# Optimization experiments

Hardware: AMD Instinct MI355X
Metric: run time of the kernel (lower is better)

## Reference

```python
import jax, jax.numpy as jnp
import numpy as np
import math

B, C, H, W = 8, 64, 256, 256
E, NH = 256, 8
HD = E // NH  # 32


def get_coords(h, w):
    xx, yy = jnp.meshgrid(jnp.arange(h, dtype=jnp.float32), jnp.arange(w, dtype=jnp.float32), indexing='ij')
    return jnp.stack((xx.reshape(-1), yy.reshape(-1)), axis=-1)  # [N, 2]


def setup_inputs() -> dict:
    key = jax.random.key(0)
    ks = jax.random.split(key, 12)
    def xavier(k, shape):
        fan_out, fan_in = shape
        a = math.sqrt(6.0 / (fan_in + fan_out))
        return jax.random.uniform(k, shape, jnp.float32, -a, a)
    x = jax.random.normal(ks[0], (B, C, H, W), jnp.float32)
    z = jax.random.normal(ks[1], (B, C), jnp.float32)
    pos = jax.random.uniform(ks[2], (B, NH, 2), jnp.float32) * (H - 1)
    Wq = xavier(ks[3], (E, C)); bq = jnp.zeros((E,), jnp.float32)
    Wk = xavier(ks[4], (E, C)); bk = jnp.zeros((E,), jnp.float32)
    Wv = xavier(ks[5], (E, C)); bv = jnp.zeros((E,), jnp.float32)
    Wp = xavier(ks[6], (HD, 2)); bp = jax.random.uniform(ks[7], (HD,), jnp.float32, -1.0, 1.0) / math.sqrt(2.0)
    return {"x": x, "z": z, "pos": pos, "Wq": Wq, "bq": bq, "Wk": Wk, "bk": bk,
            "Wv": Wv, "bv": bv, "Wp": Wp, "bp": bp}


def reference(x, z, pos, Wq, bq, Wk, bk, Wv, bv, Wp, bp):
    b, c, h, w = x.shape
    n = h * w
    x_flat = x.reshape(b, c, n).transpose(0, 2, 1)          # [B, N, C]
    pos_grid = get_coords(h, w)                              # [N, 2]
    q = (z @ Wq.T + bq).reshape(b, NH, HD)                   # [B, H, hd]
    k = (x_flat @ Wk.T + bk).reshape(b, n, NH, HD)           # [B, N, H, hd]
    # relative-position modulation of keys
    rel = pos_grid[None, :, None, :] - pos[:, None, :, :]    # [B, N, H, 2]
    qxk = rel @ Wp.T + bp                                    # [B, N, H, hd]
    k = k * qxk
    v = x_flat @ Wv.T + bv                                   # [B, N, E]
    attn_logits = jnp.einsum('bhc,bnhc->bnh', q, k) / math.sqrt(HD)
    attention = jax.nn.softmax(attn_logits, axis=1)          # softmax over N
    pos_out = jnp.einsum('bnh,nx->bhx', attention, pos_grid) # [B, H, 2]
    values = jnp.einsum('bnh,bnc->bhc', attention, v)        # [B, H, E]
    return (values, pos_out)
```

## Files before the change

kernel.cpp:

```cpp
#include <hip/hip_runtime.h>

#define NN    65536
#define NSUB  128
#define NBLK  (NN/NSUB)

typedef short bf16x8 __attribute__((ext_vector_type(8)));
typedef float f32x4v __attribute__((ext_vector_type(4)));
typedef unsigned short ushort_t;
typedef unsigned int uint_t;

#define XSTR   72
#define XHI_B  0
#define XLO_B  18432
#define LGA_B  18432
#define LGSTR  28
#define PSTR   136
#define RED_B  36864
#define SMEM_BYTES 37056

#define WTHI_B  0
#define WTLO_B  32768
#define CJ_B    65536
#define PM_B    66304
#define PL_B    197376
#define PSP_B   328448
#define PSX_B   590592
#define Q_B     8979200
#define QSTR    68

__device__ __forceinline__ uint_t bf16_rne_bits(float f) {
  uint_t u = __float_as_uint(f);
  return (u + 0x7FFFu + ((u >> 16) & 1u)) >> 16;
}
template <int CTRL>
__device__ __forceinline__ float dpp_add(float x) {
  int t = __builtin_amdgcn_update_dpp(0, __float_as_int(x), CTRL, 0xf, 0xf, false);
  return x + __int_as_float(t);
}
template <int CTRL>
__device__ __forceinline__ float dpp_maxs(float x) {
  int t = __builtin_amdgcn_update_dpp((int)0xFF800000u, __float_as_int(x), CTRL, 0xf, 0xf, false);
  return fmaxf(x, __int_as_float(t));
}
__device__ __forceinline__ float wave_sum(float x) {
  x = dpp_add<0x111>(x); x = dpp_add<0x112>(x); x = dpp_add<0x114>(x);
  x = dpp_add<0x118>(x); x = dpp_add<0x142>(x); x = dpp_add<0x143>(x);
  return __int_as_float(__builtin_amdgcn_readlane(__float_as_int(x), 63));
}
__device__ __forceinline__ float wave_max(float x) {
  x = dpp_maxs<0x111>(x); x = dpp_maxs<0x112>(x); x = dpp_maxs<0x114>(x);
  x = dpp_maxs<0x118>(x); x = dpp_maxs<0x142>(x); x = dpp_maxs<0x143>(x);
  return __int_as_float(__builtin_amdgcn_readlane(__float_as_int(x), 63));
}

__global__ __launch_bounds__(64) void prep_kernel(
    const float* __restrict__ z,  const float* __restrict__ Wq, const float* __restrict__ bq,
    const float* __restrict__ Wk, const float* __restrict__ bk,
    const float* __restrict__ Wp, const float* __restrict__ bp,
    ushort_t* __restrict__ WThi, ushort_t* __restrict__ WTlo, float* __restrict__ Cj)
{
  const int h = blockIdx.x, b = blockIdx.y, t = threadIdx.x;
  __shared__ float q[32];
  if (t < 32) {
    const int e = h*32 + t;
    float a = bq[e];
    const float* zr = z + b*64;
    const float* wr = Wq + e*64;
    #pragma unroll 8
    for (int c = 0; c < 64; ++c) a += zr[c]*wr[c];
    q[t] = a;
  }
  __syncthreads();
  const int c = t;
  float w[3] = {0.f, 0.f, 0.f};
  #pragma unroll 4
  for (int hd = 0; hd < 32; ++hd) {
    const float qk = q[hd] * Wk[(h*32+hd)*64 + c];
    w[0] += qk * bp[hd];
    w[1] += qk * Wp[hd*2+0];
    w[2] += qk * Wp[hd*2+1];
  }
  #pragma unroll
  for (int j = 0; j < 3; ++j) {
    const int coeff = h*3 + j;
    const uint_t hb = bf16_rne_bits(w[j]);
    const float  fh = __uint_as_float(hb << 16);
    const uint_t lb = bf16_rne_bits(w[j] - fh);
    WThi[(b*32 + coeff)*64 + c] = (ushort_t)hb;
    WTlo[(b*32 + coeff)*64 + c] = (ushort_t)lb;
  }
  if (h == 0) {
    #pragma unroll
    for (int r = 0; r < 8; ++r) {
      WThi[(b*32 + 24 + r)*64 + c] = 0;
      WTlo[(b*32 + 24 + r)*64 + c] = 0;
    }
  }
  if (t < 3) {
    float s = 0.f;
    for (int hd = 0; hd < 32; ++hd) {
      const float m = (t == 0) ? bp[hd] : Wp[hd*2 + (t-1)];
      s += q[hd] * m * bk[h*32+hd];
    }
    Cj[b*24 + h*3 + t] = s;
  }
}

__global__ __launch_bounds__(128, 2) void main_kernel(
    const float* __restrict__ x, const float* __restrict__ pos,
    const ushort_t* __restrict__ WThi, const ushort_t* __restrict__ WTlo,
    const float* __restrict__ Cj,
    float* __restrict__ Pm, float* __restrict__ Pl,
    float* __restrict__ Psp, float* __restrict__ Psx)
{
  extern __shared__ char smc[];
  ushort_t* xhi = (ushort_t*)(smc + XHI_B);
  float*    lga = (float*)(smc + LGA_B);
  float*    red = (float*)(smc + RED_B);
  const int t   = threadIdx.x;
  const int blk = blockIdx.x;
  const int b   = blockIdx.y;
  const int n0  = blk * NSUB;
  const int wid = t >> 6, lid = t & 63;
  const int c0  = lid & 15, q4 = lid >> 4;

  bf16x8 bh[2][2], bl[2][2];
  {
    const ushort_t* wtb_h = WThi + b*2048;
    const ushort_t* wtb_l = WTlo + b*2048;
    #pragma unroll
    for (int nt = 0; nt < 2; ++nt)
      #pragma unroll
      for (int ks = 0; ks < 2; ++ks) {
        const int off = (nt*16 + c0)*64 + ks*32 + q4*8;
        bh[nt][ks] = *(const bf16x8*)(wtb_h + off);
        bl[nt][ks] = *(const bf16x8*)(wtb_l + off);
      }
  }

  {
    const float* xg = x + (size_t)b*64*NN + n0 + t;
    float v[64];
    #pragma unroll
    for (int i = 0; i < 64; ++i) v[i] = xg[(size_t)i*NN];
    #pragma unroll
    for (int cc = 0; cc < 4; ++cc) {
      uint_t hb[16], lb[16];
      #pragma unroll
      for (int i = 0; i < 16; ++i) {
        const float f = v[cc*16+i];
        hb[i] = bf16_rne_bits(f);
        lb[i] = __float_as_uint(f - __uint_as_float(hb[i] << 16)) >> 16;
      }
      uint4 H0 = make_uint4(hb[0]|(hb[1]<<16), hb[2]|(hb[3]<<16), hb[4]|(hb[5]<<16), hb[6]|(hb[7]<<16));
      uint4 H1 = make_uint4(hb[8]|(hb[9]<<16), hb[10]|(hb[11]<<16), hb[12]|(hb[13]<<16), hb[14]|(hb[15]<<16));
      uint4 L0 = make_uint4(lb[0]|(lb[1]<<16), lb[2]|(lb[3]<<16), lb[4]|(lb[5]<<16), lb[6]|(lb[7]<<16));
      uint4 L1 = make_uint4(lb[8]|(lb[9]<<16), lb[10]|(lb[11]<<16), lb[12]|(lb[13]<<16), lb[14]|(lb[15]<<16));
      char* dh = smc + XHI_B + t*144 + cc*32;
      char* dl = smc + XLO_B + t*144 + cc*32;
      *(uint4*)(dh)      = H0;  *(uint4*)(dh + 16) = H1;
      *(uint4*)(dl)      = L0;  *(uint4*)(dl + 16) = L1;
    }
  }

  float cj[24];
  {
    const float* cjp = Cj + b*24;
    #pragma unroll
    for (int k = 0; k < 24; ++k) cj[k] = cjp[k];
  }
  const int gx = blk >> 1;
  float rxh[8], py[8];
  #pragma unroll
  for (int h = 0; h < 8; ++h) {
    rxh[h] = (float)gx - pos[(b*8+h)*2 + 0];
    py[h]  = pos[(b*8+h)*2 + 1];
  }

  __syncthreads();

  f32x4v acc[4][2];
  #pragma unroll
  for (int mt = 0; mt < 4; ++mt) { acc[mt][0] = (f32x4v)0.f; acc[mt][1] = (f32x4v)0.f; }
  {
    const int mrow0 = wid*64;
    #pragma unroll
    for (int mt = 0; mt < 4; ++mt) {
      const int row = mrow0 + mt*16 + c0;
      const ushort_t* ph = xhi + row*XSTR + q4*8;
      const ushort_t* pl = (ushort_t*)(smc + XLO_B) + row*XSTR + q4*8;
      bf16x8 ah0 = *(const bf16x8*)(ph);
      bf16x8 ah1 = *(const bf16x8*)(ph + 32);
      bf16x8 al0 = *(const bf16x8*)(pl);
      bf16x8 al1 = *(const bf16x8*)(pl + 32);
      #pragma unroll
      for (int nt = 0; nt < 2; ++nt) {
        f32x4v a = acc[mt][nt];
        a = __builtin_amdgcn_mfma_f32_16x16x32_bf16(ah0, bh[nt][0], a, 0, 0, 0);
        a = __builtin_amdgcn_mfma_f32_16x16x32_bf16(ah1, bh[nt][1], a, 0, 0, 0);
        a = __builtin_amdgcn_mfma_f32_16x16x32_bf16(ah0, bl[nt][0], a, 0, 0, 0);
        a = __builtin_amdgcn_mfma_f32_16x16x32_bf16(ah1, bl[nt][1], a, 0, 0, 0);
        a = __builtin_amdgcn_mfma_f32_16x16x32_bf16(al0, bh[nt][0], a, 0, 0, 0);
        a = __builtin_amdgcn_mfma_f32_16x16x32_bf16(al1, bh[nt][1], a, 0, 0, 0);
        acc[mt][nt] = a;
      }
    }
  }
  __syncthreads();

  {
    const int mrow0 = wid*64;
    #pragma unroll
    for (int mt = 0; mt < 4; ++mt)
      #pragma unroll
      for (int r = 0; r < 4; ++r) {
        const int prow = mrow0 + mt*16 + q4*4 + r;
        lga[prow*LGSTR + c0] = acc[mt][0][r];
        if (c0 < 8) lga[prow*LGSTR + 16 + c0] = acc[mt][1][r];
      }
  }
  __syncthreads();

  float a24[24];
  {
    const float4* ap = (const float4*)(lga + t*LGSTR);
    #pragma unroll
    for (int r = 0; r < 6; ++r) *(float4*)(a24 + 4*r) = ap[r];
  }
  const float tf = (float)(((blk & 1) << 7) + t);
  float lg[8];
  #pragma unroll
  for (int h = 0; h < 8; ++h) {
    const float a0 = a24[h*3+0] + cj[h*3+0];
    const float a1 = a24[h*3+1] + cj[h*3+1];
    const float a2 = a24[h*3+2] + cj[h*3+2];
    lg[h] = (a0 + rxh[h]*a1 + (tf - py[h])*a2) * 0.17677669529663687f;
  }

  #pragma unroll
  for (int h = 0; h < 8; ++h) {
    const float m = wave_max(lg[h]);
    if (lid == 0) red[h*2 + wid] = m;
  }
  __syncthreads();

  float p[8];
  #pragma unroll
  for (int h = 0; h < 8; ++h) {
    const float M = fmaxf(red[h*2+0], red[h*2+1]);
    p[h] = __expf(lg[h] - M);
  }

  {
    ushort_t* pls = (ushort_t*)(smc + LGA_B);
    #pragma unroll
    for (int h = 0; h < 8; ++h) {
      const uint_t hb = bf16_rne_bits(p[h]);
      const float  hf = __uint_as_float(hb << 16);
      const uint_t lb = __float_as_uint(p[h] - hf) >> 16;
      pls[h*PSTR + t]       = (ushort_t)hb;
      pls[(h+8)*PSTR + t]   = (ushort_t)lb;
    }
  }

  #pragma unroll
  for (int h = 0; h < 8; ++h) {
    const float sp  = wave_sum(p[h]);
    const float spj = wave_sum(p[h] * tf);
    if (lid == 0) { red[16 + h*2 + wid] = sp; red[32 + h*2 + wid] = spj; }
  }
  __syncthreads();

  if (t < 8) {
    const int base = (b*NBLK + blk)*8 + t;
    const float M  = fmaxf(red[t*2+0], red[t*2+1]);
    const float L  = red[16+t*2+0] + red[16+t*2+1];
    const float SJ = red[32+t*2+0] + red[32+t*2+1];
    Pm[base] = M;
    Pl[base] = L;
    Psp[base*2+0] = (float)gx * L;
    Psp[base*2+1] = SJ;
  }

  {
    const ushort_t* pls = (const ushort_t*)(smc + LGA_B);
    bf16x8 afr[4];
    #pragma unroll
    for (int ks = 0; ks < 4; ++ks)
      afr[ks] = *(const bf16x8*)(pls + c0*PSTR + ks*32 + q4*8);

    f32x4v accB0 = (f32x4v)0.f, accB1 = (f32x4v)0.f;
    const int chbase = wid*32 + c0;
    #pragma unroll
    for (int ks = 0; ks < 4; ++ks) {
      const ushort_t* xcol = xhi + (ks*32 + q4*8)*XSTR + chbase;
      bf16x8 b0, b1;
      #pragma unroll
      for (int i = 0; i < 8; ++i) {
        b0[i] = (short)xcol[i*XSTR];
        b1[i] = (short)xcol[i*XSTR + 16];
      }
      accB0 = __builtin_amdgcn_mfma_f32_16x16x32_bf16(afr[ks], b0, accB0, 0, 0, 0);
      accB1 = __builtin_amdgcn_mfma_f32_16x16x32_bf16(afr[ks], b1, accB1, 0, 0, 0);
    }

    const size_t pb64 = ((size_t)(b*NBLK + blk))*8*64;
    #pragma unroll
    for (int r = 0; r < 4; ++r) {
      const float o0 = __shfl_xor(accB0[r], 32, 64);
      const float o1 = __shfl_xor(accB1[r], 32, 64);
      if (q4 < 2) {
        const int h = q4*4 + r;
        const int c = wid*32 + c0;
        Psx[pb64 + h*64 + c]      = accB0[r] + o0;
        Psx[pb64 + h*64 + c + 16] = accB1[r] + o1;
      }
    }
  }
}

__global__ __launch_bounds__(256) void reduce1_kernel(
    const float* __restrict__ Pm, const float* __restrict__ Pl,
    const float* __restrict__ Psp, const float* __restrict__ Psx,
    float* __restrict__ Q)
{
  const int g = blockIdx.x, h = blockIdx.y, b = blockIdx.z, t = threadIdx.x;
  __shared__ float al[64];
  __shared__ float mgs;
  __shared__ float sums[3];
  __shared__ float sxl[256];
  const int base = (b*NBLK + g*64)*8 + h;

  float m_t = -1e30f;
  if (t < 64) {
    m_t = Pm[base + t*8];
    float mm = m_t;
    #pragma unroll
    for (int off = 32; off >= 1; off >>= 1) mm = fmaxf(mm, __shfl_xor(mm, off, 64));
    if (t == 0) mgs = mm;
  }
  __syncthreads();
  const float Mg = mgs;
  if (t < 64) {
    const float a = __expf(m_t - Mg);
    al[t] = a;
    float lt = Pl[base + t*8] * a;
    float sx = Psp[(base + t*8)*2 + 0] * a;
    float sy = Psp[(base + t*8)*2 + 1] * a;
    #pragma unroll
    for (int off = 32; off >= 1; off >>= 1) {
      lt += __shfl_xor(lt, off, 64);
      sx += __shfl_xor(sx, off, 64);
      sy += __shfl_xor(sy, off, 64);
    }
    if (t == 0) { sums[0] = lt; sums[1] = sx; sums[2] = sy; }
  }
  __syncthreads();
  {
    const int c = t & 63, g2 = t >> 6;
    float acc = 0.f;
    #pragma unroll
    for (int i = 0; i < 16; ++i) {
      const int k = g2*16 + i;
      acc += al[k] * Psx[(size_t)(base + k*8)*64 + c];
    }
    sxl[g2*64 + c] = acc;
  }
  __syncthreads();
  float* q = Q + ((b*8 + h)*8 + g)*QSTR;
  if (t < 64) q[4+t] = sxl[t] + sxl[64+t] + sxl[128+t] + sxl[192+t];
  if (t == 0) { q[0] = Mg; q[1] = sums[0]; q[2] = sums[1]; q[3] = sums[2]; }
}

__global__ __launch_bounds__(64) void reduce2_kernel(
    const float* __restrict__ Q, const float* __restrict__ Wv, const float* __restrict__ bv,
    float* __restrict__ out)
{
  const int h = blockIdx.x, b = blockIdx.y, t = threadIdx.x;
  __shared__ float qm[8], bl[8], l8[8], sx8[8], sy8[8];
  __shared__ float SXs[64];
  const float* qb = Q + ((b*8 + h)*8)*QSTR;

  if (t < 8) qm[t] = qb[t*QSTR + 0];
  __syncthreads();
  float M = qm[0];
  #pragma unroll
  for (int g = 1; g < 8; ++g) M = fmaxf(M, qm[g]);
  if (t < 8) {
    const float be = __expf(qm[t] - M);
    bl[t]  = be;
    l8[t]  = be * qb[t*QSTR + 1];
    sx8[t] = be * qb[t*QSTR + 2];
    sy8[t] = be * qb[t*QSTR + 3];
  }
  __syncthreads();
  float L = 0.f;
  #pragma unroll
  for (int g = 0; g < 8; ++g) L += l8[g];
  const float invL = 1.0f / L;
  {
    float s = 0.f;
    #pragma unroll
    for (int g = 0; g < 8; ++g) s += bl[g] * qb[g*QSTR + 4 + t];
    SXs[t] = s * invL;
  }
  __syncthreads();

  #pragma unroll
  for (int r = 0; r < 4; ++r) {
    const int e = t + 64*r;
    float v = bv[e];
    const float* wvr = Wv + e*64;
    #pragma unroll 8
    for (int c = 0; c < 64; ++c) v += wvr[c] * SXs[c];
    out[(b*8 + h)*256 + e] = v;
  }
  if (t == 0) {
    float spx = 0.f, spy = 0.f;
    #pragma unroll
    for (int g = 0; g < 8; ++g) { spx += sx8[g]; spy += sy8[g]; }
    out[16384 + (b*8 + h)*2 + 0] = spx * invL;
    out[16384 + (b*8 + h)*2 + 1] = spy * invL;
  }
}

extern "C" void kernel_launch(void* const* d_in, const int* in_sizes, int n_in,
                              void* d_out, int out_size, void* d_ws, size_t ws_size,
                              hipStream_t stream)
{
  const float* x   = (const float*)d_in[0];
  const float* z   = (const float*)d_in[1];
  const float* pos = (const float*)d_in[2];
  const float* Wq  = (const float*)d_in[3];
  const float* bq  = (const float*)d_in[4];
  const float* Wk  = (const float*)d_in[5];
  const float* bk  = (const float*)d_in[6];
  const float* Wv  = (const float*)d_in[7];
  const float* bv  = (const float*)d_in[8];
  const float* Wp  = (const float*)d_in[9];
  const float* bp  = (const float*)d_in[10];
  float* out = (float*)d_out;
  char*  wsb = (char*)d_ws;

  ushort_t* WThi = (ushort_t*)(wsb + WTHI_B);
  ushort_t* WTlo = (ushort_t*)(wsb + WTLO_B);
  float* Cj  = (float*)(wsb + CJ_B);
  float* Pm  = (float*)(wsb + PM_B);
  float* Pl  = (float*)(wsb + PL_B);
  float* Psp = (float*)(wsb + PSP_B);
  float* Psx = (float*)(wsb + PSX_B);
  float* Q   = (float*)(wsb + Q_B);

  prep_kernel   <<<dim3(8,8),    64,  0,          stream>>>(z, Wq, bq, Wk, bk, Wp, bp, WThi, WTlo, Cj);
  main_kernel   <<<dim3(NBLK,8), 128, SMEM_BYTES, stream>>>(x, pos, WThi, WTlo, Cj, Pm, Pl, Psp, Psx);
  reduce1_kernel<<<dim3(8,8,8),  256, 0,          stream>>>(Pm, Pl, Psp, Psx, Q);
  reduce2_kernel<<<dim3(8,8),    64,  0,          stream>>>(Q, Wv, bv, out);
}
```

Measured before the change: 237.7 us.

## Split main kernel work across 256 threads per block instead of 128

Doubles the threads per block of the main kernel. Each pixel's 64 channels are now loaded by two threads, each covering 32 channels, and the four waves split the GEMM rows, the heads and the output channel tiles between them. This cuts per-thread register pressure (64 loaded floats become 32) and raises the number of loads in flight, to hide the latency of the strided global reads of x. The launch bound now requests 4 blocks of 256, which caps registers per thread and could cause spills.

```diff
diff --git a/kernel.cpp b/kernel.cpp
--- a/kernel.cpp
+++ b/kernel.cpp
@@ -106,7 +106,7 @@
   }
 }
 
-__global__ __launch_bounds__(128, 2) void main_kernel(
+__global__ __launch_bounds__(256, 4) void main_kernel(
     const float* __restrict__ x, const float* __restrict__ pos,
     const ushort_t* __restrict__ WThi, const ushort_t* __restrict__ WTlo,
     const float* __restrict__ Cj,
@@ -123,6 +123,9 @@
   const int n0  = blk * NSUB;
   const int wid = t >> 6, lid = t & 63;
   const int c0  = lid & 15, q4 = lid >> 4;
+  const int px  = t & 127;
+  const int hgrp = t >> 7;
+  const int half = wid & 1;
 
   bf16x8 bh[2][2], bl[2][2];
   {
@@ -139,12 +142,12 @@
   }
 
   {
-    const float* xg = x + (size_t)b*64*NN + n0 + t;
-    float v[64];
-    #pragma unroll
-    for (int i = 0; i < 64; ++i) v[i] = xg[(size_t)i*NN];
-    #pragma unroll
-    for (int cc = 0; cc < 4; ++cc) {
+    const float* xg = x + (size_t)b*64*NN + (size_t)hgrp*32*NN + n0 + px;
+    float v[32];
+    #pragma unroll
+    for (int i = 0; i < 32; ++i) v[i] = xg[(size_t)i*NN];
+    #pragma unroll
+    for (int cc = 0; cc < 2; ++cc) {
       uint_t hb[16], lb[16];
       #pragma unroll
       for (int i = 0; i < 16; ++i) {
@@ -156,36 +159,37 @@
       uint4 H1 = make_uint4(hb[8]|(hb[9]<<16), hb[10]|(hb[11]<<16), hb[12]|(hb[13]<<16), hb[14]|(hb[15]<<16));
       uint4 L0 = make_uint4(lb[0]|(lb[1]<<16), lb[2]|(lb[3]<<16), lb[4]|(lb[5]<<16), lb[6]|(lb[7]<<16));
       uint4 L1 = make_uint4(lb[8]|(lb[9]<<16), lb[10]|(lb[11]<<16), lb[12]|(lb[13]<<16), lb[14]|(lb[15]<<16));
-      char* dh = smc + XHI_B + t*144 + cc*32;
-      char* dl = smc + XLO_B + t*144 + cc*32;
+      char* dh = smc + XHI_B + px*144 + (hgrp*2+cc)*32;
+      char* dl = smc + XLO_B + px*144 + (hgrp*2+cc)*32;
       *(uint4*)(dh)      = H0;  *(uint4*)(dh + 16) = H1;
       *(uint4*)(dl)      = L0;  *(uint4*)(dl + 16) = L1;
     }
   }
 
-  float cj[24];
-  {
-    const float* cjp = Cj + b*24;
-    #pragma unroll
-    for (int k = 0; k < 24; ++k) cj[k] = cjp[k];
+  float cj[12];
+  {
+    const float* cjp = Cj + b*24 + hgrp*12;
+    #pragma unroll
+    for (int k = 0; k < 12; ++k) cj[k] = cjp[k];
   }
   const int gx = blk >> 1;
-  float rxh[8], py[8];
-  #pragma unroll
-  for (int h = 0; h < 8; ++h) {
-    rxh[h] = (float)gx - pos[(b*8+h)*2 + 0];
-    py[h]  = pos[(b*8+h)*2 + 1];
-  }
-
-  __syncthreads();
-
-  f32x4v acc[4][2];
-  #pragma unroll
-  for (int mt = 0; mt < 4; ++mt) { acc[mt][0] = (f32x4v)0.f; acc[mt][1] = (f32x4v)0.f; }
-  {
-    const int mrow0 = wid*64;
-    #pragma unroll
-    for (int mt = 0; mt < 4; ++mt) {
+  float rxh[4], py[4];
+  #pragma unroll
+  for (int hl = 0; hl < 4; ++hl) {
+    const int h = hgrp*4 + hl;
+    rxh[hl] = (float)gx - pos[(b*8+h)*2 + 0];
+    py[hl]  = pos[(b*8+h)*2 + 1];
+  }
+
+  __syncthreads();
+
+  f32x4v acc[2][2];
+  #pragma unroll
+  for (int mt = 0; mt < 2; ++mt) { acc[mt][0] = (f32x4v)0.f; acc[mt][1] = (f32x4v)0.f; }
+  {
+    const int mrow0 = wid*32;
+    #pragma unroll
+    for (int mt = 0; mt < 2; ++mt) {
       const int row = mrow0 + mt*16 + c0;
       const ushort_t* ph = xhi + row*XSTR + q4*8;
       const ushort_t* pl = (ushort_t*)(smc + XLO_B) + row*XSTR + q4*8;
@@ -209,9 +213,9 @@
   __syncthreads();
 
   {
-    const int mrow0 = wid*64;
-    #pragma unroll
-    for (int mt = 0; mt < 4; ++mt)
+    const int mrow0 = wid*32;
+    #pragma unroll
+    for (int mt = 0; mt < 2; ++mt)
       #pragma unroll
       for (int r = 0; r < 4; ++r) {
         const int prow = mrow0 + mt*16 + q4*4 + r;
@@ -221,53 +225,56 @@
   }
   __syncthreads();
 
-  float a24[24];
-  {
-    const float4* ap = (const float4*)(lga + t*LGSTR);
-    #pragma unroll
-    for (int r = 0; r < 6; ++r) *(float4*)(a24 + 4*r) = ap[r];
-  }
-  const float tf = (float)(((blk & 1) << 7) + t);
-  float lg[8];
-  #pragma unroll
-  for (int h = 0; h < 8; ++h) {
-    const float a0 = a24[h*3+0] + cj[h*3+0];
-    const float a1 = a24[h*3+1] + cj[h*3+1];
-    const float a2 = a24[h*3+2] + cj[h*3+2];
-    lg[h] = (a0 + rxh[h]*a1 + (tf - py[h])*a2) * 0.17677669529663687f;
-  }
-
-  #pragma unroll
-  for (int h = 0; h < 8; ++h) {
-    const float m = wave_max(lg[h]);
-    if (lid == 0) red[h*2 + wid] = m;
-  }
-  __syncthreads();
-
-  float p[8];
-  #pragma unroll
-  for (int h = 0; h < 8; ++h) {
+  float a12[12];
+  {
+    const float4* ap = (const float4*)(lga + px*LGSTR + hgrp*12);
+    #pragma unroll
+    for (int r = 0; r < 3; ++r) *(float4*)(a12 + 4*r) = ap[r];
+  }
+  const float tf = (float)(((blk & 1) << 7) + px);
+  float lg[4];
+  #pragma unroll
+  for (int hl = 0; hl < 4; ++hl) {
+    const float a0 = a12[hl*3+0] + cj[hl*3+0];
+    const float a1 = a12[hl*3+1] + cj[hl*3+1];
+    const float a2 = a12[hl*3+2] + cj[hl*3+2];
+    lg[hl] = (a0 + rxh[hl]*a1 + (tf - py[hl])*a2) * 0.17677669529663687f;
+  }
+
+  #pragma unroll
+  for (int hl = 0; hl < 4; ++hl) {
+    const float m = wave_max(lg[hl]);
+    if (lid == 0) red[(hgrp*4 + hl)*2 + half] = m;
+  }
+  __syncthreads();
+
+  float p[4];
+  #pragma unroll
+  for (int hl = 0; hl < 4; ++hl) {
+    const int h = hgrp*4 + hl;
     const float M = fmaxf(red[h*2+0], red[h*2+1]);
-    p[h] = __expf(lg[h] - M);
+    p[hl] = __expf(lg[hl] - M);
   }
 
   {
     ushort_t* pls = (ushort_t*)(smc + LGA_B);
     #pragma unroll
-    for (int h = 0; h < 8; ++h) {
-      const uint_t hb = bf16_rne_bits(p[h]);
+    for (int hl = 0; hl < 4; ++hl) {
+      const int h = hgrp*4 + hl;
+      const uint_t hb = bf16_rne_bits(p[hl]);
       const float  hf = __uint_as_float(hb << 16);
-      const uint_t lb = __float_as_uint(p[h] - hf) >> 16;
-      pls[h*PSTR + t]       = (ushort_t)hb;
-      pls[(h+8)*PSTR + t]   = (ushort_t)lb;
-    }
-  }
-
-  #pragma unroll
-  for (int h = 0; h < 8; ++h) {
-    const float sp  = wave_sum(p[h]);
-    const float spj = wave_sum(p[h] * tf);
-    if (lid == 0) { red[16 + h*2 + wid] = sp; red[32 + h*2 + wid] = spj; }
+      const uint_t lb = __float_as_uint(p[hl] - hf) >> 16;
+      pls[h*PSTR + px]       = (ushort_t)hb;
+      pls[(h+8)*PSTR + px]   = (ushort_t)lb;
+    }
+  }
+
+  #pragma unroll
+  for (int hl = 0; hl < 4; ++hl) {
+    const int h = hgrp*4 + hl;
+    const float sp  = wave_sum(p[hl]);
+    const float spj = wave_sum(p[hl] * tf);
+    if (lid == 0) { red[16 + h*2 + half] = sp; red[32 + h*2 + half] = spj; }
   }
   __syncthreads();
 
@@ -289,31 +296,24 @@
     for (int ks = 0; ks < 4; ++ks)
       afr[ks] = *(const bf16x8*)(pls + c0*PSTR + ks*32 + q4*8);
 
-    f32x4v accB0 = (f32x4v)0.f, accB1 = (f32x4v)0.f;
-    const int chbase = wid*32 + c0;
+    f32x4v accB = (f32x4v)0.f;
+    const int chbase = wid*16 + c0;
     #pragma unroll
     for (int ks = 0; ks < 4; ++ks) {
       const ushort_t* xcol = xhi + (ks*32 + q4*8)*XSTR + chbase;
-      bf16x8 b0, b1;
+      bf16x8 bfr;
       #pragma unroll
-      for (int i = 0; i < 8; ++i) {
-        b0[i] = (short)xcol[i*XSTR];
-        b1[i] = (short)xcol[i*XSTR + 16];
-      }
-      accB0 = __builtin_amdgcn_mfma_f32_16x16x32_bf16(afr[ks], b0, accB0, 0, 0, 0);
-      accB1 = __builtin_amdgcn_mfma_f32_16x16x32_bf16(afr[ks], b1, accB1, 0, 0, 0);
+      for (int i = 0; i < 8; ++i) bfr[i] = (short)xcol[i*XSTR];
+      accB = __builtin_amdgcn_mfma_f32_16x16x32_bf16(afr[ks], bfr, accB, 0, 0, 0);
     }
 
     const size_t pb64 = ((size_t)(b*NBLK + blk))*8*64;
     #pragma unroll
     for (int r = 0; r < 4; ++r) {
-      const float o0 = __shfl_xor(accB0[r], 32, 64);
-      const float o1 = __shfl_xor(accB1[r], 32, 64);
+      const float o = __shfl_xor(accB[r], 32, 64);
       if (q4 < 2) {
         const int h = q4*4 + r;
-        const int c = wid*32 + c0;
-        Psx[pb64 + h*64 + c]      = accB0[r] + o0;
-        Psx[pb64 + h*64 + c + 16] = accB1[r] + o1;
+        Psx[pb64 + h*64 + chbase] = accB[r] + o;
       }
     }
   }
@@ -452,7 +452,7 @@
   float* Q   = (float*)(wsb + Q_B);
 
   prep_kernel   <<<dim3(8,8),    64,  0,          stream>>>(z, Wq, bq, Wk, bk, Wp, bp, WThi, WTlo, Cj);
-  main_kernel   <<<dim3(NBLK,8), 128, SMEM_BYTES, stream>>>(x, pos, WThi, WTlo, Cj, Pm, Pl, Psp, Psx);
+  main_kernel   <<<dim3(NBLK,8), 256, SMEM_BYTES, stream>>>(x, pos, WThi, WTlo, Cj, Pm, Pl, Psp, Psx);
   reduce1_kernel<<<dim3(8,8,8),  256, 0,          stream>>>(Pm, Pl, Psp, Psx, Q);
   reduce2_kernel<<<dim3(8,8),    64,  0,          stream>>>(Q, Wv, bv, out);
 }
```

New measurement: 234.6 us. Within noise of the previous version (-1.3%).
